# Optimization experiments

Hardware: AMD Instinct MI355X
Metric: run time of the kernel (lower is better)

## Reference

```python
import jax, jax.numpy as jnp
import numpy as np

B = 512       # number of graphs
MAX_N = 128   # pad length (>= max(num_atoms))
D = 256       # emb_dim


def setup_inputs() -> dict:
    key = jax.random.key(0)
    ks = jax.random.split(key, 20)
    num_atoms_np = np.full(B, 80, dtype=np.int64)
    num_atoms_np[: B // 2] = 112
    num_atoms_np[B // 2 :] = 48
    total = int(num_atoms_np.sum())  # 40960, static
    scale = 1.0 / np.sqrt(D)

    def lin_w(k):
        return jax.random.normal(k, (D, D), jnp.float32) * scale

    inp = {
        'rep_2d': jax.random.normal(ks[0], (total, D), jnp.float32),
        'rep_3d': jax.random.normal(ks[1], (total, D), jnp.float32),
        'num_atoms': jnp.asarray(num_atoms_np),
        # mha_2d_3d (queries from 2d, keys/values from 3d)
        'wq23': lin_w(ks[2]), 'bq23': jnp.zeros((D,), jnp.float32),
        'wk23': lin_w(ks[3]), 'bk23': jnp.zeros((D,), jnp.float32),
        'wv23': lin_w(ks[4]), 'bv23': jnp.zeros((D,), jnp.float32),
        # mha_3d_2d (queries from 3d, keys/values from 2d)
        'wq32': lin_w(ks[5]), 'bq32': jnp.zeros((D,), jnp.float32),
        'wk32': lin_w(ks[6]), 'bk32': jnp.zeros((D,), jnp.float32),
        'wv32': lin_w(ks[7]), 'bv32': jnp.zeros((D,), jnp.float32),
        # per-branch Linear (normalizer=Identity) + GELU
        'wm23': lin_w(ks[8]), 'bm23': jnp.zeros((D,), jnp.float32),
        'wm32': lin_w(ks[9]), 'bm32': jnp.zeros((D,), jnp.float32),
    }
    return inp


def _variadic_to_padded(flat, num_atoms):
    # flat: [total, D] -> padded [B, MAX_N, D], mask [B, MAX_N] (True = valid)
    cum = jnp.cumsum(num_atoms)
    offsets = cum - num_atoms
    pos = jnp.arange(MAX_N)
    mask = pos[None, :] < num_atoms[:, None]
    idx = jnp.where(mask, offsets[:, None] + pos[None, :], 0)
    padded = flat[idx] * mask[..., None].astype(flat.dtype)
    return padded, mask


def _padded_to_variadic(padded, num_atoms, total):
    # padded: [B, MAX_N, D] -> flat [total, D]
    cum = jnp.cumsum(num_atoms)
    t = jnp.arange(total)
    b = jnp.searchsorted(cum, t, side='right')
    i = t - (cum - num_atoms)[b]
    return padded[b, i]


def _cross_attn(q_in, kv_in, mask, wq, bq, wk, bk, wv, bv):
    # single-head scaled dot-product cross-attention, key-side padding mask
    q = q_in @ wq.T + bq
    k = kv_in @ wk.T + bk
    v = kv_in @ wv.T + bv
    s = jnp.einsum('bqd,bkd->bqk', q, k) / jnp.sqrt(jnp.asarray(D, q.dtype))
    s = jnp.where(mask[:, None, :], s, jnp.asarray(-1e9, s.dtype))
    a = jax.nn.softmax(s, axis=-1)
    return jnp.einsum('bqk,bkd->bqd', a, v)


def reference(rep_2d, rep_3d, num_atoms,
              wq23, bq23, wk23, bk23, wv23, bv23,
              wq32, bq32, wk32, bk32, wv32, bv32,
              wm23, bm23, wm32, bm32):
    total = rep_2d.shape[0]
    p2d, mask = _variadic_to_padded(rep_2d, num_atoms)
    p3d, _ = _variadic_to_padded(rep_3d, num_atoms)
    x2d = _cross_attn(p2d, p3d, mask, wq23, bq23, wk23, bk23, wv23, bv23)
    x3d = _cross_attn(p3d, p2d, mask, wq32, bq32, wk32, bk32, wv32, bv32)
    x2d = _padded_to_variadic(x2d, num_atoms, total)
    x3d = _padded_to_variadic(x3d, num_atoms, total)
    out2d = jax.nn.gelu(x2d @ wm23.T + bm23, approximate=False)
    out3d = jax.nn.gelu(x3d @ wm32.T + bm32, approximate=False)
    return (out2d, out3d)
```

## Files before the change

### kernel.cpp

```cpp
#include <hip/hip_runtime.h>
#include <hip/hip_bf16.h>
#include <cstdint>


typedef short s16x8 __attribute__((ext_vector_type(8)));
typedef float f32x4 __attribute__((ext_vector_type(4)));

__device__ __forceinline__ s16x8 cvt8(const float* p) {
  float4 a0 = *(const float4*)p, a1 = *(const float4*)(p + 4);
  union { s16x8 v; __bf16 e[8]; } u;
  u.e[0] = (__bf16)a0.x; u.e[1] = (__bf16)a0.y; u.e[2] = (__bf16)a0.z; u.e[3] = (__bf16)a0.w;
  u.e[4] = (__bf16)a1.x; u.e[5] = (__bf16)a1.y; u.e[6] = (__bf16)a1.z; u.e[7] = (__bf16)a1.w;
  return u.v;
}
__device__ __forceinline__ float fast_gelu(float x) {
  float ax = fabsf(x);
  float t = 1.0f / (1.0f + 0.3275911f * (ax * 0.70710678f));
  float y = t * (0.254829592f + t * (-0.284496736f + t * (1.421413741f +
            t * (-1.453152027f + t * 1.061405429f))));
  float er = 1.0f - y * __expf(-0.5f * ax * ax);
  er = (x < 0.f) ? -er : er;
  return 0.5f * x * (1.0f + er);
}

__global__ void sentinel_kernel(float* out, float v) {
  if (threadIdx.x == 0 && blockIdx.x == 0) out[0] = v;
}

__global__ __launch_bounds__(512) void scan_kernel(
    const int* __restrict__ na, int* __restrict__ offs,
    int B, int total, float* out)
{
  __shared__ int s32[512];
  __shared__ int s64[512];
  const int t = threadIdx.x;
  int v32 = 0, v64 = 0;
  if (t < B) {
    v32 = na[t];
    v64 = (int)((const long long*)na)[t];
  }
  s32[t] = v32; s64[t] = v64;
  __syncthreads();
  for (int o = 1; o < 512; o <<= 1) {
    int a = (t >= o) ? s32[t - o] : 0;
    int b = (t >= o) ? s64[t - o] : 0;
    __syncthreads();
    s32[t] += a; s64[t] += b;
    __syncthreads();
  }
  int tot32 = s32[B - 1], tot64 = s64[B - 1];
  bool ok32 = (tot32 == total), ok64 = (tot64 == total);
  if (t < B) offs[t] = ok32 ? (s32[t] - v32) : ok64 ? (s64[t] - v64) : 0;
  if (t == 0) {
    offs[B] = ok32 ? tot32 : ok64 ? tot64 : 0;
    if (!ok32 && !ok64) out[0] = 31337.0f;
  }
}

__global__ __launch_bounds__(256) void qkv_fused(
    const float* __restrict__ A,
    const float* __restrict__ Wq, const float* __restrict__ bq,
    const float* __restrict__ Wk, const float* __restrict__ bk,
    const float* __restrict__ Wv, const float* __restrict__ bv,
    __bf16* __restrict__ Qo, __bf16* __restrict__ Ko, __bf16* __restrict__ Vt,
    int total)
{
  __shared__ __bf16 Al[64][264];
  __shared__ __bf16 Wt[128][40];
  const int t = threadIdx.x, lane = t & 63, w = t >> 6;
  const int wr = w >> 1, wc = w & 1;
  const int l15 = lane & 15, l4 = lane >> 4;
  const int by = blockIdx.x;

  #pragma unroll
  for (int j = 0; j < 8; ++j) {
    int c = t + j * 256;
    int row = c >> 5, off0 = (c & 31) * 8;
    *(s16x8*)(&Al[row][off0]) = cvt8(A + (size_t)(by * 64 + row) * 256 + off0);
  }
  __syncthreads();

  #pragma unroll
  for (int wi = 0; wi < 3; ++wi) {
    const float* W  = (wi == 0) ? Wq : (wi == 1) ? Wk : Wv;
    const float* bs = (wi == 0) ? bq : (wi == 1) ? bk : bv;
    #pragma unroll
    for (int nx = 0; nx < 2; ++nx) {
      f32x4 acc[2][4];
      #pragma unroll
      for (int m = 0; m < 2; ++m)
        #pragma unroll
        for (int nn = 0; nn < 4; ++nn) acc[m][nn] = (f32x4){0.f, 0.f, 0.f, 0.f};

      for (int kk = 0; kk < 256; kk += 32) {
        __syncthreads();
        #pragma unroll
        for (int j = 0; j < 2; ++j) {
          int c = t + j * 256;
          int row = c >> 2, off0 = (c & 3) * 8;
          *(s16x8*)(&Wt[row][off0]) =
              cvt8(W + (size_t)(nx * 128 + row) * 256 + kk + off0);
        }
        __syncthreads();
        s16x8 af[2], bfr[4];
        #pragma unroll
        for (int m = 0; m < 2; ++m)
          af[m] = *(const s16x8*)(&Al[wr * 32 + m * 16 + l15][kk + l4 * 8]);
        #pragma unroll
        for (int nn = 0; nn < 4; ++nn)
          bfr[nn] = *(const s16x8*)(&Wt[wc * 64 + nn * 16 + l15][l4 * 8]);
        #pragma unroll
        for (int m = 0; m < 2; ++m)
          #pragma unroll
          for (int nn = 0; nn < 4; ++nn)
            acc[m][nn] = __builtin_amdgcn_mfma_f32_16x16x32_bf16(af[m], bfr[nn], acc[m][nn], 0, 0, 0);
      }

      if (wi < 2) {
        __bf16* O = (wi == 0) ? Qo : Ko;
        #pragma unroll
        for (int m = 0; m < 2; ++m) {
          int row0 = by * 64 + wr * 32 + m * 16 + l4 * 4;
          #pragma unroll
          for (int nn = 0; nn < 4; ++nn) {
            int col = nx * 128 + wc * 64 + nn * 16 + l15;
            float bc = bs[col];
            #pragma unroll
            for (int r = 0; r < 4; ++r)
              O[(size_t)(row0 + r) * 256 + col] = (__bf16)(acc[m][nn][r] + bc);
          }
        }
      } else {
        #pragma unroll
        for (int m = 0; m < 2; ++m) {
          int row0 = by * 64 + wr * 32 + m * 16 + l4 * 4;
          #pragma unroll
          for (int nn = 0; nn < 4; ++nn) {
            int col = nx * 128 + wc * 64 + nn * 16 + l15;
            float bc = bs[col];
            union { uint2 u; __bf16 e[4]; } pv;
            #pragma unroll
            for (int r = 0; r < 4; ++r) pv.e[r] = (__bf16)(acc[m][nn][r] + bc);
            *(uint2*)(&Vt[(size_t)col * total + row0]) = pv.u;
          }
        }
      }
    }
  }
}

__global__ __launch_bounds__(256) void gemm_kernel(
    const float* __restrict__ A, const float* __restrict__ Bw,
    const float* __restrict__ bias, __bf16* __restrict__ C,
    int N, int biasRow)
{
  __shared__ __bf16 At[128 * 32];
  __shared__ __bf16 Bt[128 * 32];
  const int t = threadIdx.x;
  const int lane = t & 63, w = t >> 6;
  const int wr = w >> 1, wc = w & 1;
  const int l15 = lane & 15, l4 = lane >> 4;
  const int by = blockIdx.x, bx = blockIdx.y;

  f32x4 acc[4][4];
  for (int m = 0; m < 4; ++m)
    for (int nn = 0; nn < 4; ++nn) acc[m][nn] = (f32x4){0.f, 0.f, 0.f, 0.f};

  for (int kk = 0; kk < 256; kk += 32) {
    for (int j = 0; j < 2; ++j) {
      int c = t + j * 256;
      int row = c >> 2, off0 = (c & 3) * 8;
      *(s16x8*)(&At[row * 32 + off0]) = cvt8(A + (size_t)(by * 128 + row) * 256 + kk + off0);
      *(s16x8*)(&Bt[row * 32 + off0]) = cvt8(Bw + (size_t)(bx * 128 + row) * 256 + kk + off0);
    }
    __syncthreads();
    s16x8 af[4], bfr[4];
    for (int m = 0; m < 4; ++m)
      af[m] = *(const s16x8*)(&At[(wr * 64 + m * 16 + l15) * 32 + l4 * 8]);
    for (int nn = 0; nn < 4; ++nn)
      bfr[nn] = *(const s16x8*)(&Bt[(wc * 64 + nn * 16 + l15) * 32 + l4 * 8]);
    for (int m = 0; m < 4; ++m)
      for (int nn = 0; nn < 4; ++nn)
        acc[m][nn] = __builtin_amdgcn_mfma_f32_16x16x32_bf16(af[m], bfr[nn], acc[m][nn], 0, 0, 0);
    __syncthreads();
  }

  for (int m = 0; m < 4; ++m) {
    int row0 = by * 128 + wr * 64 + m * 16 + l4 * 4;
    for (int nn = 0; nn < 4; ++nn) {
      int col = bx * 128 + wc * 64 + nn * 16 + l15;
      float bc = biasRow ? 0.f : bias[col];
      for (int r = 0; r < 4; ++r) {
        int row = row0 + r;
        float v = acc[m][nn][r] + (biasRow ? bias[row] : bc);
        C[(size_t)row * N + col] = (__bf16)v;
      }
    }
  }
}

__global__ __launch_bounds__(256) void gemm_out(
    const __bf16* __restrict__ A, const float* __restrict__ Bw,
    const float* __restrict__ bias, float* __restrict__ C, int N)
{
  __shared__ __bf16 At[64 * 32];
  __shared__ __bf16 Bt[128 * 32];
  const int t = threadIdx.x;
  const int lane = t & 63, w = t >> 6;
  const int wr = w >> 1, wc = w & 1;
  const int l15 = lane & 15, l4 = lane >> 4;
  const int by = blockIdx.x, bx = blockIdx.y;

  f32x4 acc[2][4];
  for (int m = 0; m < 2; ++m)
    for (int nn = 0; nn < 4; ++nn) acc[m][nn] = (f32x4){0.f, 0.f, 0.f, 0.f};

  for (int kk = 0; kk < 256; kk += 32) {
    {
      int row = t >> 2, off0 = (t & 3) * 8;
      *(s16x8*)(&At[row * 32 + off0]) =
          *(const s16x8*)(A + (size_t)(by * 64 + row) * 256 + kk + off0);
    }
    for (int j = 0; j < 2; ++j) {
      int c = t + j * 256;
      int row = c >> 2, off0 = (c & 3) * 8;
      *(s16x8*)(&Bt[row * 32 + off0]) = cvt8(Bw + (size_t)(bx * 128 + row) * 256 + kk + off0);
    }
    __syncthreads();
    s16x8 af[2], bfr[4];
    for (int m = 0; m < 2; ++m)
      af[m] = *(const s16x8*)(&At[(wr * 32 + m * 16 + l15) * 32 + l4 * 8]);
    for (int nn = 0; nn < 4; ++nn)
      bfr[nn] = *(const s16x8*)(&Bt[(wc * 64 + nn * 16 + l15) * 32 + l4 * 8]);
    for (int m = 0; m < 2; ++m)
      for (int nn = 0; nn < 4; ++nn)
        acc[m][nn] = __builtin_amdgcn_mfma_f32_16x16x32_bf16(af[m], bfr[nn], acc[m][nn], 0, 0, 0);
    __syncthreads();
  }

  for (int m = 0; m < 2; ++m) {
    int row0 = by * 64 + wr * 32 + m * 16 + l4 * 4;
    for (int nn = 0; nn < 4; ++nn) {
      int col = bx * 128 + wc * 64 + nn * 16 + l15;
      float bc = bias[col];
      for (int r = 0; r < 4; ++r) {
        int row = row0 + r;
        C[(size_t)row * N + col] = fast_gelu(acc[m][nn][r] + bc);
      }
    }
  }
}

#define KSTR 264
#define PSTR 136
__global__ __launch_bounds__(512, 2) void attn_kernel(
    const __bf16* __restrict__ Q, const __bf16* __restrict__ Km,
    const __bf16* __restrict__ Vt, __bf16* __restrict__ X,
    const int* __restrict__ offs, int total)
{
  __shared__ __bf16 smem[128 * KSTR];
  __bf16 (*Klds)[KSTR] = (__bf16(*)[KSTR])smem;
  __bf16 (*Plds)[PSTR] = (__bf16(*)[PSTR])smem;

  const int g = blockIdx.x;
  const int off = offs[g];
  const int n = offs[g + 1] - off;
  const int t = threadIdx.x, lane = t & 63, w = t >> 6;
  const int l15 = lane & 15, l4 = lane >> 4;
  const bool qact = (w * 16) < n;

  uint4 kst[8];
  #pragma unroll
  for (int j = 0; j < 8; ++j) {
    int row = j * 16 + (t >> 5);
    kst[j] = *(const uint4*)((const char*)(Km + (size_t)(off + row) * 256) + (t & 31) * 16);
  }
  s16x8 qf[8];
  if (qact) {
    int qr = w * 16 + l15; if (qr >= n) qr = n - 1;
    const __bf16* qp = Q + (size_t)(off + qr) * 256 + l4 * 8;
    #pragma unroll
    for (int kk = 0; kk < 8; ++kk) qf[kk] = *(const s16x8*)(qp + kk * 32);
  }
  #pragma unroll
  for (int j = 0; j < 8; ++j) {
    int row = j * 16 + (t >> 5);
    *(uint4*)((char*)&Klds[row][0] + (t & 31) * 16) = kst[j];
  }
  __syncthreads();

  f32x4 sacc[8];
  #pragma unroll
  for (int i = 0; i < 8; ++i) sacc[i] = (f32x4){0.f, 0.f, 0.f, 0.f};
  if (qact) {
    #pragma unroll
    for (int kt = 0; kt < 8; ++kt) {
      if (kt * 16 < n) {
        const __bf16* kp = &Klds[kt * 16 + l15][l4 * 8];
        #pragma unroll
        for (int kk = 0; kk < 8; ++kk) {
          s16x8 kf = *(const s16x8*)(kp + kk * 32);
          sacc[kt] = __builtin_amdgcn_mfma_f32_16x16x32_bf16(qf[kk], kf, sacc[kt], 0, 0, 0);
        }
      }
    }
  }
  __syncthreads();

  if (qact) {
    #pragma unroll
    for (int r = 0; r < 4; ++r) {
      float sv[8];
      float m = -1e30f;
      #pragma unroll
      for (int kt = 0; kt < 8; ++kt) {
        int key = kt * 16 + l15;
        float v = (key < n) ? sacc[kt][r] * 0.0625f : -1e30f;
        sv[kt] = v; m = fmaxf(m, v);
      }
      for (int o = 1; o < 16; o <<= 1) m = fmaxf(m, __shfl_xor(m, o));
      float p[8], sum = 0.f;
      #pragma unroll
      for (int kt = 0; kt < 8; ++kt) { p[kt] = __expf(sv[kt] - m); sum += p[kt]; }
      for (int o = 1; o < 16; o <<= 1) sum += __shfl_xor(sum, o);
      float inv = 1.f / sum;
      int q = w * 16 + l4 * 4 + r;
      #pragma unroll
      for (int kt = 0; kt < 8; ++kt)
        Plds[q][kt * 16 + l15] = (__bf16)(p[kt] * inv);
    }
  }
  __syncthreads();

  const int dbase = w * 32;
  f32x4 xacc[2][8];
  #pragma unroll
  for (int dt = 0; dt < 2; ++dt)
    #pragma unroll
    for (int qm = 0; qm < 8; ++qm) xacc[dt][qm] = (f32x4){0.f, 0.f, 0.f, 0.f};

  #pragma unroll
  for (int dt = 0; dt < 2; ++dt) {
    int d = dbase + dt * 16 + l15;
    s16x8 vf[4];
    #pragma unroll
    for (int ks = 0; ks < 4; ++ks) {
      int kc = off + ks * 32 + l4 * 8;
      if (kc > total - 8) kc = total - 8;
      vf[ks] = *(const s16x8*)(Vt + (size_t)d * total + kc);
    }
    #pragma unroll
    for (int qm = 0; qm < 8; ++qm) {
      #pragma unroll
      for (int ks = 0; ks < 4; ++ks) {
        if (ks * 32 < n) {
          s16x8 pa = *(const s16x8*)(&Plds[qm * 16 + l15][ks * 32 + l4 * 8]);
          xacc[dt][qm] = __builtin_amdgcn_mfma_f32_16x16x32_bf16(pa, vf[ks], xacc[dt][qm], 0, 0, 0);
        }
      }
    }
  }

  #pragma unroll
  for (int dt = 0; dt < 2; ++dt)
    #pragma unroll
    for (int qm = 0; qm < 8; ++qm)
      #pragma unroll
      for (int r = 0; r < 4; ++r) {
        int q = qm * 16 + l4 * 4 + r;
        if (q < n)
          X[(size_t)(off + q) * 256 + dbase + dt * 16 + l15] = (__bf16)xacc[dt][qm][r];
      }
}

extern "C" void kernel_launch(void* const* d_in, const int* in_sizes, int n_in,
                              void* d_out, int out_size, void* d_ws, size_t ws_size,
                              hipStream_t stream) {
  const float* rep2d = (const float*)d_in[0];
  const float* rep3d = (const float*)d_in[1];
  const int*   na    = (const int*)d_in[2];
  const float* wq23 = (const float*)d_in[3];  const float* bq23 = (const float*)d_in[4];
  const float* wk23 = (const float*)d_in[5];  const float* bk23 = (const float*)d_in[6];
  const float* wv23 = (const float*)d_in[7];  const float* bv23 = (const float*)d_in[8];
  const float* wq32 = (const float*)d_in[9];  const float* bq32 = (const float*)d_in[10];
  const float* wk32 = (const float*)d_in[11]; const float* bk32 = (const float*)d_in[12];
  const float* wv32 = (const float*)d_in[13]; const float* bv32 = (const float*)d_in[14];
  const float* wm23 = (const float*)d_in[15]; const float* bm23 = (const float*)d_in[16];
  const float* wm32 = (const float*)d_in[17]; const float* bm32 = (const float*)d_in[18];

  const int B = in_sizes[2];
  const int total = in_sizes[0] / 256;
  float* out = (float*)d_out;

  char* ws = (char*)d_ws;
  const size_t SZ = (size_t)total * 256 * sizeof(__bf16);
  const size_t need6 = 8192 + 6 * SZ;
  const size_t need3 = 8192 + 3 * SZ;
  int* offs = (int*)ws;

  dim3 blk(256);
  dim3 gO(total / 64, 2);
  dim3 gA(B);
  dim3 blkA(512);

  if (ws_size >= need6) {
    __bf16* BQ1 = (__bf16*)(ws + 8192);
    __bf16* BK1 = (__bf16*)(ws + 8192 + SZ);
    __bf16* BV1 = (__bf16*)(ws + 8192 + 2 * SZ);
    __bf16* BQ2 = (__bf16*)(ws + 8192 + 3 * SZ);
    __bf16* BK2 = (__bf16*)(ws + 8192 + 4 * SZ);
    __bf16* BV2 = (__bf16*)(ws + 8192 + 5 * SZ);

    scan_kernel<<<1, 512, 0, stream>>>(na, offs, B, total, out);
    qkv_fused<<<total / 64, blk, 0, stream>>>(rep2d, wq23, bq23, wk32, bk32,
                                              wv32, bv32, BQ1, BK2, BV2, total);
    qkv_fused<<<total / 64, blk, 0, stream>>>(rep3d, wq32, bq32, wk23, bk23,
                                              wv23, bv23, BQ2, BK1, BV1, total);
    attn_kernel<<<gA, blkA, 0, stream>>>(BQ1, BK1, BV1, BQ1, offs, total);
    gemm_out<<<gO, blk, 0, stream>>>(BQ1, wm23, bm23, out, 256);
    attn_kernel<<<gA, blkA, 0, stream>>>(BQ2, BK2, BV2, BQ2, offs, total);
    gemm_out<<<gO, blk, 0, stream>>>(BQ2, wm32, bm32, out + (size_t)total * 256, 256);
  } else if (ws_size >= need3) {
    __bf16* BQ = (__bf16*)(ws + 8192);
    __bf16* BK = (__bf16*)(ws + 8192 + SZ);
    __bf16* BV = (__bf16*)(ws + 8192 + 2 * SZ);
    dim3 gP(total / 128, 2);
    dim3 gV(2, total / 128);

    scan_kernel<<<1, 512, 0, stream>>>(na, offs, B, total, out);
    gemm_kernel<<<gP, blk, 0, stream>>>(rep2d, wq23, bq23, BQ, 256, 0);
    gemm_kernel<<<gP, blk, 0, stream>>>(rep3d, wk23, bk23, BK, 256, 0);
    gemm_kernel<<<gV, blk, 0, stream>>>(wv23, rep3d, bv23, BV, total, 1);
    attn_kernel<<<gA, blkA, 0, stream>>>(BQ, BK, BV, BQ, offs, total);
    gemm_out<<<gO, blk, 0, stream>>>(BQ, wm23, bm23, out, 256);
    gemm_kernel<<<gP, blk, 0, stream>>>(rep3d, wq32, bq32, BQ, 256, 0);
    gemm_kernel<<<gP, blk, 0, stream>>>(rep2d, wk32, bk32, BK, 256, 0);
    gemm_kernel<<<gV, blk, 0, stream>>>(wv32, rep2d, bv32, BV, total, 1);
    attn_kernel<<<gA, blkA, 0, stream>>>(BQ, BK, BV, BQ, offs, total);
    gemm_out<<<gO, blk, 0, stream>>>(BQ, wm32, bm32, out + (size_t)total * 256, 256);
  } else {
    sentinel_kernel<<<1, 64, 0, stream>>>(out, 54321.0f);
  }
}
```

Before: 216.0 us.

## Pre-convert QKV weights to bf16 and load MFMA fragments directly from global

Adds a small kernel that converts the six QKV weight matrices to bf16 once per call into workspace. The QKV kernel drops its shared-memory staging. Activation fragments are converted straight into registers, and weight fragments are read directly from the bf16 global copy, which removes the per-k-step barriers and repeated fp32-to-bf16 conversion of weights in every block. The trade is one extra launch, more register pressure, and uncoalesced-ish 16-byte global loads for weights that now rely on L2/cache instead of LDS.

```diff
diff --git a/kernel.cpp b/kernel.cpp
--- a/kernel.cpp
+++ b/kernel.cpp
@@ -57,32 +57,44 @@
   }
 }
 
+__global__ __launch_bounds__(256) void cvt6_kernel(
+    const float* __restrict__ w0, const float* __restrict__ w1,
+    const float* __restrict__ w2, const float* __restrict__ w3,
+    const float* __restrict__ w4, const float* __restrict__ w5,
+    __bf16* __restrict__ out)
+{
+  const int wi = blockIdx.y;
+  const float* w = (wi == 0) ? w0 : (wi == 1) ? w1 : (wi == 2) ? w2
+                 : (wi == 3) ? w3 : (wi == 4) ? w4 : w5;
+  int i = (blockIdx.x * 256 + threadIdx.x) * 4;
+  float4 f = *(const float4*)(w + i);
+  __bf16* o = out + (size_t)wi * 65536 + i;
+  o[0] = (__bf16)f.x; o[1] = (__bf16)f.y; o[2] = (__bf16)f.z; o[3] = (__bf16)f.w;
+}
+
 __global__ __launch_bounds__(256) void qkv_fused(
-    const float* __restrict__ A,
-    const float* __restrict__ Wq, const float* __restrict__ bq,
-    const float* __restrict__ Wk, const float* __restrict__ bk,
-    const float* __restrict__ Wv, const float* __restrict__ bv,
+    const float* __restrict__ A, const __bf16* __restrict__ Wb,
+    const float* __restrict__ bq, const float* __restrict__ bk,
+    const float* __restrict__ bv,
     __bf16* __restrict__ Qo, __bf16* __restrict__ Ko, __bf16* __restrict__ Vt,
     int total)
 {
-  __shared__ __bf16 Al[64][264];
-  __shared__ __bf16 Wt[128][40];
   const int t = threadIdx.x, lane = t & 63, w = t >> 6;
   const int wr = w >> 1, wc = w & 1;
   const int l15 = lane & 15, l4 = lane >> 4;
   const int by = blockIdx.x;
 
-  #pragma unroll
-  for (int j = 0; j < 8; ++j) {
-    int c = t + j * 256;
-    int row = c >> 5, off0 = (c & 31) * 8;
-    *(s16x8*)(&Al[row][off0]) = cvt8(A + (size_t)(by * 64 + row) * 256 + off0);
-  }
-  __syncthreads();
+  s16x8 afr[2][8];
+  #pragma unroll
+  for (int m = 0; m < 2; ++m) {
+    const float* ap = A + (size_t)(by * 64 + wr * 32 + m * 16 + l15) * 256 + l4 * 8;
+    #pragma unroll
+    for (int kk = 0; kk < 8; ++kk) afr[m][kk] = cvt8(ap + kk * 32);
+  }
 
   #pragma unroll
   for (int wi = 0; wi < 3; ++wi) {
-    const float* W  = (wi == 0) ? Wq : (wi == 1) ? Wk : Wv;
+    const __bf16* W  = Wb + (size_t)wi * 65536;
     const float* bs = (wi == 0) ? bq : (wi == 1) ? bk : bv;
     #pragma unroll
     for (int nx = 0; nx < 2; ++nx) {
@@ -92,28 +104,18 @@
         #pragma unroll
         for (int nn = 0; nn < 4; ++nn) acc[m][nn] = (f32x4){0.f, 0.f, 0.f, 0.f};
 
-      for (int kk = 0; kk < 256; kk += 32) {
-        __syncthreads();
-        #pragma unroll
-        for (int j = 0; j < 2; ++j) {
-          int c = t + j * 256;
-          int row = c >> 2, off0 = (c & 3) * 8;
-          *(s16x8*)(&Wt[row][off0]) =
-              cvt8(W + (size_t)(nx * 128 + row) * 256 + kk + off0);
-        }
-        __syncthreads();
-        s16x8 af[2], bfr[4];
-        #pragma unroll
-        for (int m = 0; m < 2; ++m)
-          af[m] = *(const s16x8*)(&Al[wr * 32 + m * 16 + l15][kk + l4 * 8]);
+      #pragma unroll
+      for (int kk = 0; kk < 8; ++kk) {
+        s16x8 wf[4];
         #pragma unroll
         for (int nn = 0; nn < 4; ++nn)
-          bfr[nn] = *(const s16x8*)(&Wt[wc * 64 + nn * 16 + l15][l4 * 8]);
+          wf[nn] = *(const s16x8*)(W + (size_t)(nx * 128 + wc * 64 + nn * 16 + l15) * 256
+                                    + kk * 32 + l4 * 8);
         #pragma unroll
         for (int m = 0; m < 2; ++m)
           #pragma unroll
           for (int nn = 0; nn < 4; ++nn)
-            acc[m][nn] = __builtin_amdgcn_mfma_f32_16x16x32_bf16(af[m], bfr[nn], acc[m][nn], 0, 0, 0);
+            acc[m][nn] = __builtin_amdgcn_mfma_f32_16x16x32_bf16(afr[m][kk], wf[nn], acc[m][nn], 0, 0, 0);
       }
 
       if (wi < 2) {
@@ -394,7 +396,8 @@
 
   char* ws = (char*)d_ws;
   const size_t SZ = (size_t)total * 256 * sizeof(__bf16);
-  const size_t need6 = 8192 + 6 * SZ;
+  const size_t WB = 6 * 65536 * sizeof(__bf16);
+  const size_t need6 = 8192 + WB + 6 * SZ;
   const size_t need3 = 8192 + 3 * SZ;
   int* offs = (int*)ws;
 
@@ -404,18 +407,20 @@
   dim3 blkA(512);
 
   if (ws_size >= need6) {
-    __bf16* BQ1 = (__bf16*)(ws + 8192);
-    __bf16* BK1 = (__bf16*)(ws + 8192 + SZ);
-    __bf16* BV1 = (__bf16*)(ws + 8192 + 2 * SZ);
-    __bf16* BQ2 = (__bf16*)(ws + 8192 + 3 * SZ);
-    __bf16* BK2 = (__bf16*)(ws + 8192 + 4 * SZ);
-    __bf16* BV2 = (__bf16*)(ws + 8192 + 5 * SZ);
+    __bf16* WBp = (__bf16*)(ws + 8192);
+    __bf16* BQ1 = (__bf16*)(ws + 8192 + WB);
+    __bf16* BK1 = (__bf16*)(ws + 8192 + WB + SZ);
+    __bf16* BV1 = (__bf16*)(ws + 8192 + WB + 2 * SZ);
+    __bf16* BQ2 = (__bf16*)(ws + 8192 + WB + 3 * SZ);
+    __bf16* BK2 = (__bf16*)(ws + 8192 + WB + 4 * SZ);
+    __bf16* BV2 = (__bf16*)(ws + 8192 + WB + 5 * SZ);
 
     scan_kernel<<<1, 512, 0, stream>>>(na, offs, B, total, out);
-    qkv_fused<<<total / 64, blk, 0, stream>>>(rep2d, wq23, bq23, wk32, bk32,
-                                              wv32, bv32, BQ1, BK2, BV2, total);
-    qkv_fused<<<total / 64, blk, 0, stream>>>(rep3d, wq32, bq32, wk23, bk23,
-                                              wv23, bv23, BQ2, BK1, BV1, total);
+    cvt6_kernel<<<dim3(64, 6), blk, 0, stream>>>(wq23, wk32, wv32, wq32, wk23, wv23, WBp);
+    qkv_fused<<<total / 64, blk, 0, stream>>>(rep2d, WBp, bq23, bk32, bv32,
+                                              BQ1, BK2, BV2, total);
+    qkv_fused<<<total / 64, blk, 0, stream>>>(rep3d, WBp + 3 * 65536, bq32, bk23, bv23,
+                                              BQ2, BK1, BV1, total);
     attn_kernel<<<gA, blkA, 0, stream>>>(BQ1, BK1, BV1, BQ1, offs, total);
     gemm_out<<<gO, blk, 0, stream>>>(BQ1, wm23, bm23, out, 256);
     attn_kernel<<<gA, blkA, 0, stream>>>(BQ2, BK2, BV2, BQ2, offs, total);
```

Result: slower. 274.5 us (+27.1%).

## Batch both branches into single projection, attention, and output launches

Applied to the files above, without the earlier changes.

Replaces the two per-input fused QKV kernels with one 3D-grid projection kernel that runs all six Q/K/V GEMMs as independent 128x128 tiles. The attention and output GEMMs for both branches are merged into single launches indexed by blockIdx.y/z. The aim is fewer launches, more blocks in flight per launch, and no serialization between the two branches. In exchange, the A-tile reuse across Q/K/V in the old fused kernel is lost: each input tile is reloaded and reconverted for every projection, and the grid includes early-exit blocks.

```diff
diff --git a/kernel.cpp b/kernel.cpp
--- a/kernel.cpp
+++ b/kernel.cpp
@@ -57,93 +57,253 @@
   }
 }
 
-__global__ __launch_bounds__(256) void qkv_fused(
-    const float* __restrict__ A,
-    const float* __restrict__ Wq, const float* __restrict__ bq,
-    const float* __restrict__ Wk, const float* __restrict__ bk,
-    const float* __restrict__ Wv, const float* __restrict__ bv,
-    __bf16* __restrict__ Qo, __bf16* __restrict__ Ko, __bf16* __restrict__ Vt,
-    int total)
+struct Proj6Args {
+  const float* A[6]; const float* W[6]; const float* bias[6];
+  unsigned long long C[6];
+};
+__global__ __launch_bounds__(256) void proj6_kernel(Proj6Args args, int total)
 {
-  __shared__ __bf16 Al[64][264];
-  __shared__ __bf16 Wt[128][40];
-  const int t = threadIdx.x, lane = t & 63, w = t >> 6;
+  __shared__ __bf16 At[128 * 32];
+  __shared__ __bf16 Bt[128 * 32];
+  const int z = blockIdx.z;
+  const bool vcase = (z == 2 || z == 5);
+  const float* A  = args.A[z];
+  const float* Bw = args.W[z];
+  const float* bs = args.bias[z];
+  __bf16* C = (__bf16*)args.C[z];
+  const int N = vcase ? total : 256;
+  const int by = vcase ? blockIdx.y : blockIdx.x;
+  const int bx = vcase ? blockIdx.x : blockIdx.y;
+  if (vcase && blockIdx.x >= (unsigned)(total / 128)) return;
+  if (!vcase && blockIdx.y >= 2) return;
+
+  const int t = threadIdx.x;
+  const int lane = t & 63, w = t >> 6;
   const int wr = w >> 1, wc = w & 1;
   const int l15 = lane & 15, l4 = lane >> 4;
-  const int by = blockIdx.x;
-
+
+  f32x4 acc[4][4];
+  for (int m = 0; m < 4; ++m)
+    for (int nn = 0; nn < 4; ++nn) acc[m][nn] = (f32x4){0.f, 0.f, 0.f, 0.f};
+
+  for (int kk = 0; kk < 256; kk += 32) {
+    for (int j = 0; j < 2; ++j) {
+      int c = t + j * 256;
+      int row = c >> 2, off0 = (c & 3) * 8;
+      *(s16x8*)(&At[row * 32 + off0]) = cvt8(A + (size_t)(by * 128 + row) * 256 + kk + off0);
+      *(s16x8*)(&Bt[row * 32 + off0]) = cvt8(Bw + (size_t)(bx * 128 + row) * 256 + kk + off0);
+    }
+    __syncthreads();
+    s16x8 af[4], bfr[4];
+    for (int m = 0; m < 4; ++m)
+      af[m] = *(const s16x8*)(&At[(wr * 64 + m * 16 + l15) * 32 + l4 * 8]);
+    for (int nn = 0; nn < 4; ++nn)
+      bfr[nn] = *(const s16x8*)(&Bt[(wc * 64 + nn * 16 + l15) * 32 + l4 * 8]);
+    for (int m = 0; m < 4; ++m)
+      for (int nn = 0; nn < 4; ++nn)
+        acc[m][nn] = __builtin_amdgcn_mfma_f32_16x16x32_bf16(af[m], bfr[nn], acc[m][nn], 0, 0, 0);
+    __syncthreads();
+  }
+
+  for (int m = 0; m < 4; ++m) {
+    int row0 = by * 128 + wr * 64 + m * 16 + l4 * 4;
+    for (int nn = 0; nn < 4; ++nn) {
+      int col = bx * 128 + wc * 64 + nn * 16 + l15;
+      float bc = vcase ? 0.f : bs[col];
+      for (int r = 0; r < 4; ++r) {
+        int row = row0 + r;
+        float v = acc[m][nn][r] + (vcase ? bs[row] : bc);
+        C[(size_t)row * N + col] = (__bf16)v;
+      }
+    }
+  }
+}
+
+struct Attn2Args {
+  const __bf16* Q[2]; const __bf16* K[2]; const __bf16* V[2];
+  unsigned long long X[2];
+};
+#define KSTR 264
+#define PSTR 136
+__global__ __launch_bounds__(512, 2) void attn2_kernel(
+    Attn2Args args, const int* __restrict__ offs, int total)
+{
+  __shared__ __bf16 smem[128 * KSTR];
+  __bf16 (*Klds)[KSTR] = (__bf16(*)[KSTR])smem;
+  __bf16 (*Plds)[PSTR] = (__bf16(*)[PSTR])smem;
+
+  const int br = blockIdx.y;
+  const __bf16* Q  = args.Q[br];
+  const __bf16* Km = args.K[br];
+  const __bf16* Vt = args.V[br];
+  __bf16* X = (__bf16*)args.X[br];
+
+  const int g = blockIdx.x;
+  const int off = offs[g];
+  const int n = offs[g + 1] - off;
+  const int t = threadIdx.x, lane = t & 63, w = t >> 6;
+  const int l15 = lane & 15, l4 = lane >> 4;
+  const bool qact = (w * 16) < n;
+
+  uint4 kst[8];
   #pragma unroll
   for (int j = 0; j < 8; ++j) {
-    int c = t + j * 256;
-    int row = c >> 5, off0 = (c & 31) * 8;
-    *(s16x8*)(&Al[row][off0]) = cvt8(A + (size_t)(by * 64 + row) * 256 + off0);
+    int row = j * 16 + (t >> 5);
+    kst[j] = *(const uint4*)((const char*)(Km + (size_t)(off + row) * 256) + (t & 31) * 16);
+  }
+  s16x8 qf[8];
+  if (qact) {
+    int qr = w * 16 + l15; if (qr >= n) qr = n - 1;
+    const __bf16* qp = Q + (size_t)(off + qr) * 256 + l4 * 8;
+    #pragma unroll
+    for (int kk = 0; kk < 8; ++kk) qf[kk] = *(const s16x8*)(qp + kk * 32);
+  }
+  #pragma unroll
+  for (int j = 0; j < 8; ++j) {
+    int row = j * 16 + (t >> 5);
+    *(uint4*)((char*)&Klds[row][0] + (t & 31) * 16) = kst[j];
   }
   __syncthreads();
 
-  #pragma unroll
-  for (int wi = 0; wi < 3; ++wi) {
-    const float* W  = (wi == 0) ? Wq : (wi == 1) ? Wk : Wv;
-    const float* bs = (wi == 0) ? bq : (wi == 1) ? bk : bv;
-    #pragma unroll
-    for (int nx = 0; nx < 2; ++nx) {
-      f32x4 acc[2][4];
+  f32x4 sacc[8];
+  #pragma unroll
+  for (int i = 0; i < 8; ++i) sacc[i] = (f32x4){0.f, 0.f, 0.f, 0.f};
+  if (qact) {
+    #pragma unroll
+    for (int kt = 0; kt < 8; ++kt) {
+      if (kt * 16 < n) {
+        const __bf16* kp = &Klds[kt * 16 + l15][l4 * 8];
+        #pragma unroll
+        for (int kk = 0; kk < 8; ++kk) {
+          s16x8 kf = *(const s16x8*)(kp + kk * 32);
+          sacc[kt] = __builtin_amdgcn_mfma_f32_16x16x32_bf16(qf[kk], kf, sacc[kt], 0, 0, 0);
+        }
+      }
+    }
+  }
+  __syncthreads();
+
+  if (qact) {
+    #pragma unroll
+    for (int r = 0; r < 4; ++r) {
+      float sv[8];
+      float m = -1e30f;
       #pragma unroll
-      for (int m = 0; m < 2; ++m)
-        #pragma unroll
-        for (int nn = 0; nn < 4; ++nn) acc[m][nn] = (f32x4){0.f, 0.f, 0.f, 0.f};
-
-      for (int kk = 0; kk < 256; kk += 32) {
-        __syncthreads();
-        #pragma unroll
-        for (int j = 0; j < 2; ++j) {
-          int c = t + j * 256;
-          int row = c >> 2, off0 = (c & 3) * 8;
-          *(s16x8*)(&Wt[row][off0]) =
-              cvt8(W + (size_t)(nx * 128 + row) * 256 + kk + off0);
+      for (int kt = 0; kt < 8; ++kt) {
+        int key = kt * 16 + l15;
+        float v = (key < n) ? sacc[kt][r] * 0.0625f : -1e30f;
+        sv[kt] = v; m = fmaxf(m, v);
+      }
+      for (int o = 1; o < 16; o <<= 1) m = fmaxf(m, __shfl_xor(m, o));
+      float p[8], sum = 0.f;
+      #pragma unroll
+      for (int kt = 0; kt < 8; ++kt) { p[kt] = __expf(sv[kt] - m); sum += p[kt]; }
+      for (int o = 1; o < 16; o <<= 1) sum += __shfl_xor(sum, o);
+      float inv = 1.f / sum;
+      int q = w * 16 + l4 * 4 + r;
+      #pragma unroll
+      for (int kt = 0; kt < 8; ++kt)
+        Plds[q][kt * 16 + l15] = (__bf16)(p[kt] * inv);
+    }
+  }
+  __syncthreads();
+
+  const int dbase = w * 32;
+  f32x4 xacc[2][8];
+  #pragma unroll
+  for (int dt = 0; dt < 2; ++dt)
+    #pragma unroll
+    for (int qm = 0; qm < 8; ++qm) xacc[dt][qm] = (f32x4){0.f, 0.f, 0.f, 0.f};
+
+  #pragma unroll
+  for (int dt = 0; dt < 2; ++dt) {
+    int d = dbase + dt * 16 + l15;
+    s16x8 vf[4];
+    #pragma unroll
+    for (int ks = 0; ks < 4; ++ks) {
+      int kc = off + ks * 32 + l4 * 8;
+      if (kc > total - 8) kc = total - 8;
+      vf[ks] = *(const s16x8*)(Vt + (size_t)d * total + kc);
+    }
+    #pragma unroll
+    for (int qm = 0; qm < 8; ++qm) {
+      #pragma unroll
+      for (int ks = 0; ks < 4; ++ks) {
+        if (ks * 32 < n) {
+          s16x8 pa = *(const s16x8*)(&Plds[qm * 16 + l15][ks * 32 + l4 * 8]);
+          xacc[dt][qm] = __builtin_amdgcn_mfma_f32_16x16x32_bf16(pa, vf[ks], xacc[dt][qm], 0, 0, 0);
         }
-        __syncthreads();
-        s16x8 af[2], bfr[4];
-        #pragma unroll
-        for (int m = 0; m < 2; ++m)
-          af[m] = *(const s16x8*)(&Al[wr * 32 + m * 16 + l15][kk + l4 * 8]);
-        #pragma unroll
-        for (int nn = 0; nn < 4; ++nn)
-          bfr[nn] = *(const s16x8*)(&Wt[wc * 64 + nn * 16 + l15][l4 * 8]);
-        #pragma unroll
-        for (int m = 0; m < 2; ++m)
-          #pragma unroll
-          for (int nn = 0; nn < 4; ++nn)
-            acc[m][nn] = __builtin_amdgcn_mfma_f32_16x16x32_bf16(af[m], bfr[nn], acc[m][nn], 0, 0, 0);
-      }
-
-      if (wi < 2) {
-        __bf16* O = (wi == 0) ? Qo : Ko;
-        #pragma unroll
-        for (int m = 0; m < 2; ++m) {
-          int row0 = by * 64 + wr * 32 + m * 16 + l4 * 4;
-          #pragma unroll
-          for (int nn = 0; nn < 4; ++nn) {
-            int col = nx * 128 + wc * 64 + nn * 16 + l15;
-            float bc = bs[col];
-            #pragma unroll
-            for (int r = 0; r < 4; ++r)
-              O[(size_t)(row0 + r) * 256 + col] = (__bf16)(acc[m][nn][r] + bc);
-          }
-        }
-      } else {
-        #pragma unroll
-        for (int m = 0; m < 2; ++m) {
-          int row0 = by * 64 + wr * 32 + m * 16 + l4 * 4;
-          #pragma unroll
-          for (int nn = 0; nn < 4; ++nn) {
-            int col = nx * 128 + wc * 64 + nn * 16 + l15;
-            float bc = bs[col];
-            union { uint2 u; __bf16 e[4]; } pv;
-            #pragma unroll
-            for (int r = 0; r < 4; ++r) pv.e[r] = (__bf16)(acc[m][nn][r] + bc);
-            *(uint2*)(&Vt[(size_t)col * total + row0]) = pv.u;
-          }
-        }
+      }
+    }
+  }
+
+  #pragma unroll
+  for (int dt = 0; dt < 2; ++dt)
+    #pragma unroll
+    for (int qm = 0; qm < 8; ++qm)
+      #pragma unroll
+      for (int r = 0; r < 4; ++r) {
+        int q = qm * 16 + l4 * 4 + r;
+        if (q < n)
+          X[(size_t)(off + q) * 256 + dbase + dt * 16 + l15] = (__bf16)xacc[dt][qm][r];
+      }
+}
+
+struct Out2Args {
+  const __bf16* A[2]; const float* W[2]; const float* bias[2];
+  unsigned long long C[2];
+};
+__global__ __launch_bounds__(256) void gemm_out2(Out2Args args)
+{
+  __shared__ __bf16 At[64 * 32];
+  __shared__ __bf16 Bt[128 * 32];
+  const int z = blockIdx.z;
+  const __bf16* A  = args.A[z];
+  const float* Bw  = args.W[z];
+  const float* bias = args.bias[z];
+  float* C = (float*)args.C[z];
+
+  const int t = threadIdx.x;
+  const int lane = t & 63, w = t >> 6;
+  const int wr = w >> 1, wc = w & 1;
+  const int l15 = lane & 15, l4 = lane >> 4;
+  const int by = blockIdx.x, bx = blockIdx.y;
+
+  f32x4 acc[2][4];
+  for (int m = 0; m < 2; ++m)
+    for (int nn = 0; nn < 4; ++nn) acc[m][nn] = (f32x4){0.f, 0.f, 0.f, 0.f};
+
+  for (int kk = 0; kk < 256; kk += 32) {
+    {
+      int row = t >> 2, off0 = (t & 3) * 8;
+      *(s16x8*)(&At[row * 32 + off0]) =
+          *(const s16x8*)(A + (size_t)(by * 64 + row) * 256 + kk + off0);
+    }
+    for (int j = 0; j < 2; ++j) {
+      int c = t + j * 256;
+      int row = c >> 2, off0 = (c & 3) * 8;
+      *(s16x8*)(&Bt[row * 32 + off0]) = cvt8(Bw + (size_t)(bx * 128 + row) * 256 + kk + off0);
+    }
+    __syncthreads();
+    s16x8 af[2], bfr[4];
+    for (int m = 0; m < 2; ++m)
+      af[m] = *(const s16x8*)(&At[(wr * 32 + m * 16 + l15) * 32 + l4 * 8]);
+    for (int nn = 0; nn < 4; ++nn)
+      bfr[nn] = *(const s16x8*)(&Bt[(wc * 64 + nn * 16 + l15) * 32 + l4 * 8]);
+    for (int m = 0; m < 2; ++m)
+      for (int nn = 0; nn < 4; ++nn)
+        acc[m][nn] = __builtin_amdgcn_mfma_f32_16x16x32_bf16(af[m], bfr[nn], acc[m][nn], 0, 0, 0);
+    __syncthreads();
+  }
+
+  for (int m = 0; m < 2; ++m) {
+    int row0 = by * 64 + wr * 32 + m * 16 + l4 * 4;
+    for (int nn = 0; nn < 4; ++nn) {
+      int col = bx * 128 + wc * 64 + nn * 16 + l15;
+      float bc = bias[col];
+      for (int r = 0; r < 4; ++r) {
+        int row = row0 + r;
+        C[(size_t)row * 256 + col] = fast_gelu(acc[m][nn][r] + bc);
       }
     }
   }
@@ -197,180 +357,6 @@
       }
     }
   }
-}
-
-__global__ __launch_bounds__(256) void gemm_out(
-    const __bf16* __restrict__ A, const float* __restrict__ Bw,
-    const float* __restrict__ bias, float* __restrict__ C, int N)
-{
-  __shared__ __bf16 At[64 * 32];
-  __shared__ __bf16 Bt[128 * 32];
-  const int t = threadIdx.x;
-  const int lane = t & 63, w = t >> 6;
-  const int wr = w >> 1, wc = w & 1;
-  const int l15 = lane & 15, l4 = lane >> 4;
-  const int by = blockIdx.x, bx = blockIdx.y;
-
-  f32x4 acc[2][4];
-  for (int m = 0; m < 2; ++m)
-    for (int nn = 0; nn < 4; ++nn) acc[m][nn] = (f32x4){0.f, 0.f, 0.f, 0.f};
-
-  for (int kk = 0; kk < 256; kk += 32) {
-    {
-      int row = t >> 2, off0 = (t & 3) * 8;
-      *(s16x8*)(&At[row * 32 + off0]) =
-          *(const s16x8*)(A + (size_t)(by * 64 + row) * 256 + kk + off0);
-    }
-    for (int j = 0; j < 2; ++j) {
-      int c = t + j * 256;
-      int row = c >> 2, off0 = (c & 3) * 8;
-      *(s16x8*)(&Bt[row * 32 + off0]) = cvt8(Bw + (size_t)(bx * 128 + row) * 256 + kk + off0);
-    }
-    __syncthreads();
-    s16x8 af[2], bfr[4];
-    for (int m = 0; m < 2; ++m)
-      af[m] = *(const s16x8*)(&At[(wr * 32 + m * 16 + l15) * 32 + l4 * 8]);
-    for (int nn = 0; nn < 4; ++nn)
-      bfr[nn] = *(const s16x8*)(&Bt[(wc * 64 + nn * 16 + l15) * 32 + l4 * 8]);
-    for (int m = 0; m < 2; ++m)
-      for (int nn = 0; nn < 4; ++nn)
-        acc[m][nn] = __builtin_amdgcn_mfma_f32_16x16x32_bf16(af[m], bfr[nn], acc[m][nn], 0, 0, 0);
-    __syncthreads();
-  }
-
-  for (int m = 0; m < 2; ++m) {
-    int row0 = by * 64 + wr * 32 + m * 16 + l4 * 4;
-    for (int nn = 0; nn < 4; ++nn) {
-      int col = bx * 128 + wc * 64 + nn * 16 + l15;
-      float bc = bias[col];
-      for (int r = 0; r < 4; ++r) {
-        int row = row0 + r;
-        C[(size_t)row * N + col] = fast_gelu(acc[m][nn][r] + bc);
-      }
-    }
-  }
-}
-
-#define KSTR 264
-#define PSTR 136
-__global__ __launch_bounds__(512, 2) void attn_kernel(
-    const __bf16* __restrict__ Q, const __bf16* __restrict__ Km,
-    const __bf16* __restrict__ Vt, __bf16* __restrict__ X,
-    const int* __restrict__ offs, int total)
-{
-  __shared__ __bf16 smem[128 * KSTR];
-  __bf16 (*Klds)[KSTR] = (__bf16(*)[KSTR])smem;
-  __bf16 (*Plds)[PSTR] = (__bf16(*)[PSTR])smem;
-
-  const int g = blockIdx.x;
-  const int off = offs[g];
-  const int n = offs[g + 1] - off;
-  const int t = threadIdx.x, lane = t & 63, w = t >> 6;
-  const int l15 = lane & 15, l4 = lane >> 4;
-  const bool qact = (w * 16) < n;
-
-  uint4 kst[8];
-  #pragma unroll
-  for (int j = 0; j < 8; ++j) {
-    int row = j * 16 + (t >> 5);
-    kst[j] = *(const uint4*)((const char*)(Km + (size_t)(off + row) * 256) + (t & 31) * 16);
-  }
-  s16x8 qf[8];
-  if (qact) {
-    int qr = w * 16 + l15; if (qr >= n) qr = n - 1;
-    const __bf16* qp = Q + (size_t)(off + qr) * 256 + l4 * 8;
-    #pragma unroll
-    for (int kk = 0; kk < 8; ++kk) qf[kk] = *(const s16x8*)(qp + kk * 32);
-  }
-  #pragma unroll
-  for (int j = 0; j < 8; ++j) {
-    int row = j * 16 + (t >> 5);
-    *(uint4*)((char*)&Klds[row][0] + (t & 31) * 16) = kst[j];
-  }
-  __syncthreads();
-
-  f32x4 sacc[8];
-  #pragma unroll
-  for (int i = 0; i < 8; ++i) sacc[i] = (f32x4){0.f, 0.f, 0.f, 0.f};
-  if (qact) {
-    #pragma unroll
-    for (int kt = 0; kt < 8; ++kt) {
-      if (kt * 16 < n) {
-        const __bf16* kp = &Klds[kt * 16 + l15][l4 * 8];
-        #pragma unroll
-        for (int kk = 0; kk < 8; ++kk) {
-          s16x8 kf = *(const s16x8*)(kp + kk * 32);
-          sacc[kt] = __builtin_amdgcn_mfma_f32_16x16x32_bf16(qf[kk], kf, sacc[kt], 0, 0, 0);
-        }
-      }
-    }
-  }
-  __syncthreads();
-
-  if (qact) {
-    #pragma unroll
-    for (int r = 0; r < 4; ++r) {
-      float sv[8];
-      float m = -1e30f;
-      #pragma unroll
-      for (int kt = 0; kt < 8; ++kt) {
-        int key = kt * 16 + l15;
-        float v = (key < n) ? sacc[kt][r] * 0.0625f : -1e30f;
-        sv[kt] = v; m = fmaxf(m, v);
-      }
-      for (int o = 1; o < 16; o <<= 1) m = fmaxf(m, __shfl_xor(m, o));
-      float p[8], sum = 0.f;
-      #pragma unroll
-      for (int kt = 0; kt < 8; ++kt) { p[kt] = __expf(sv[kt] - m); sum += p[kt]; }
-      for (int o = 1; o < 16; o <<= 1) sum += __shfl_xor(sum, o);
-      float inv = 1.f / sum;
-      int q = w * 16 + l4 * 4 + r;
-      #pragma unroll
-      for (int kt = 0; kt < 8; ++kt)
-        Plds[q][kt * 16 + l15] = (__bf16)(p[kt] * inv);
-    }
-  }
-  __syncthreads();
-
-  const int dbase = w * 32;
-  f32x4 xacc[2][8];
-  #pragma unroll
-  for (int dt = 0; dt < 2; ++dt)
-    #pragma unroll
-    for (int qm = 0; qm < 8; ++qm) xacc[dt][qm] = (f32x4){0.f, 0.f, 0.f, 0.f};
-
-  #pragma unroll
-  for (int dt = 0; dt < 2; ++dt) {
-    int d = dbase + dt * 16 + l15;
-    s16x8 vf[4];
-    #pragma unroll
-    for (int ks = 0; ks < 4; ++ks) {
-      int kc = off + ks * 32 + l4 * 8;
-      if (kc > total - 8) kc = total - 8;
-      vf[ks] = *(const s16x8*)(Vt + (size_t)d * total + kc);
-    }
-    #pragma unroll
-    for (int qm = 0; qm < 8; ++qm) {
-      #pragma unroll
-      for (int ks = 0; ks < 4; ++ks) {
-        if (ks * 32 < n) {
-          s16x8 pa = *(const s16x8*)(&Plds[qm * 16 + l15][ks * 32 + l4 * 8]);
-          xacc[dt][qm] = __builtin_amdgcn_mfma_f32_16x16x32_bf16(pa, vf[ks], xacc[dt][qm], 0, 0, 0);
-        }
-      }
-    }
-  }
-
-  #pragma unroll
-  for (int dt = 0; dt < 2; ++dt)
-    #pragma unroll
-    for (int qm = 0; qm < 8; ++qm)
-      #pragma unroll
-      for (int r = 0; r < 4; ++r) {
-        int q = qm * 16 + l4 * 4 + r;
-        if (q < n)
-          X[(size_t)(off + q) * 256 + dbase + dt * 16 + l15] = (__bf16)xacc[dt][qm][r];
-      }
 }
 
 extern "C" void kernel_launch(void* const* d_in, const int* in_sizes, int n_in,
@@ -399,8 +385,6 @@
   int* offs = (int*)ws;
 
   dim3 blk(256);
-  dim3 gO(total / 64, 2);
-  dim3 gA(B);
   dim3 blkA(512);
 
   if (ws_size >= need6) {
@@ -412,32 +396,56 @@
     __bf16* BV2 = (__bf16*)(ws + 8192 + 5 * SZ);
 
     scan_kernel<<<1, 512, 0, stream>>>(na, offs, B, total, out);
-    qkv_fused<<<total / 64, blk, 0, stream>>>(rep2d, wq23, bq23, wk32, bk32,
-                                              wv32, bv32, BQ1, BK2, BV2, total);
-    qkv_fused<<<total / 64, blk, 0, stream>>>(rep3d, wq32, bq32, wk23, bk23,
-                                              wv23, bv23, BQ2, BK1, BV1, total);
-    attn_kernel<<<gA, blkA, 0, stream>>>(BQ1, BK1, BV1, BQ1, offs, total);
-    gemm_out<<<gO, blk, 0, stream>>>(BQ1, wm23, bm23, out, 256);
-    attn_kernel<<<gA, blkA, 0, stream>>>(BQ2, BK2, BV2, BQ2, offs, total);
-    gemm_out<<<gO, blk, 0, stream>>>(BQ2, wm32, bm32, out + (size_t)total * 256, 256);
+
+    Proj6Args pa;
+    pa.A[0] = rep2d; pa.W[0] = wq23; pa.bias[0] = bq23; pa.C[0] = (unsigned long long)BQ1;
+    pa.A[1] = rep3d; pa.W[1] = wk23; pa.bias[1] = bk23; pa.C[1] = (unsigned long long)BK1;
+    pa.A[2] = wv23;  pa.W[2] = rep3d; pa.bias[2] = bv23; pa.C[2] = (unsigned long long)BV1;
+    pa.A[3] = rep3d; pa.W[3] = wq32; pa.bias[3] = bq32; pa.C[3] = (unsigned long long)BQ2;
+    pa.A[4] = rep2d; pa.W[4] = wk32; pa.bias[4] = bk32; pa.C[4] = (unsigned long long)BK2;
+    pa.A[5] = wv32;  pa.W[5] = rep2d; pa.bias[5] = bv32; pa.C[5] = (unsigned long long)BV2;
+    proj6_kernel<<<dim3(total / 128, 2, 6), blk, 0, stream>>>(pa, total);
+
+    Attn2Args aa;
+    aa.Q[0] = BQ1; aa.K[0] = BK1; aa.V[0] = BV1; aa.X[0] = (unsigned long long)BQ1;
+    aa.Q[1] = BQ2; aa.K[1] = BK2; aa.V[1] = BV2; aa.X[1] = (unsigned long long)BQ2;
+    attn2_kernel<<<dim3(B, 2), blkA, 0, stream>>>(aa, offs, total);
+
+    Out2Args oa;
+    oa.A[0] = BQ1; oa.W[0] = wm23; oa.bias[0] = bm23; oa.C[0] = (unsigned long long)out;
+    oa.A[1] = BQ2; oa.W[1] = wm32; oa.bias[1] = bm32;
+    oa.C[1] = (unsigned long long)(out + (size_t)total * 256);
+    gemm_out2<<<dim3(total / 64, 2, 2), blk, 0, stream>>>(oa);
   } else if (ws_size >= need3) {
     __bf16* BQ = (__bf16*)(ws + 8192);
     __bf16* BK = (__bf16*)(ws + 8192 + SZ);
     __bf16* BV = (__bf16*)(ws + 8192 + 2 * SZ);
     dim3 gP(total / 128, 2);
     dim3 gV(2, total / 128);
+    dim3 gA(B);
 
     scan_kernel<<<1, 512, 0, stream>>>(na, offs, B, total, out);
-    gemm_kernel<<<gP, blk, 0, stream>>>(rep2d, wq23, bq23, BQ, 256, 0);
-    gemm_kernel<<<gP, blk, 0, stream>>>(rep3d, wk23, bk23, BK, 256, 0);
-    gemm_kernel<<<gV, blk, 0, stream>>>(wv23, rep3d, bv23, BV, total, 1);
-    attn_kernel<<<gA, blkA, 0, stream>>>(BQ, BK, BV, BQ, offs, total);
-    gemm_out<<<gO, blk, 0, stream>>>(BQ, wm23, bm23, out, 256);
-    gemm_kernel<<<gP, blk, 0, stream>>>(rep3d, wq32, bq32, BQ, 256, 0);
-    gemm_kernel<<<gP, blk, 0, stream>>>(rep2d, wk32, bk32, BK, 256, 0);
-    gemm_kernel<<<gV, blk, 0, stream>>>(wv32, rep2d, bv32, BV, total, 1);
-    attn_kernel<<<gA, blkA, 0, stream>>>(BQ, BK, BV, BQ, offs, total);
-    gemm_out<<<gO, blk, 0, stream>>>(BQ, wm32, bm32, out + (size_t)total * 256, 256);
+    for (int br = 0; br < 2; ++br) {
+      const float* rq = br ? rep3d : rep2d;
+      const float* rk = br ? rep2d : rep3d;
+      const float* wq = br ? wq32 : wq23;  const float* bq = br ? bq32 : bq23;
+      const float* wk = br ? wk32 : wk23;  const float* bk = br ? bk32 : bk23;
+      const float* wv = br ? wv32 : wv23;  const float* bv = br ? bv32 : bv23;
+      const float* wm = br ? wm32 : wm23;  const float* bm = br ? bm32 : bm23;
+      float* o = out + (size_t)br * total * 256;
+
+      gemm_kernel<<<gP, blk, 0, stream>>>(rq, wq, bq, BQ, 256, 0);
+      gemm_kernel<<<gP, blk, 0, stream>>>(rk, wk, bk, BK, 256, 0);
+      gemm_kernel<<<gV, blk, 0, stream>>>(wv, rk, bv, BV, total, 1);
+      Attn2Args aa;
+      aa.Q[0] = BQ; aa.K[0] = BK; aa.V[0] = BV; aa.X[0] = (unsigned long long)BQ;
+      aa.Q[1] = BQ; aa.K[1] = BK; aa.V[1] = BV; aa.X[1] = (unsigned long long)BQ;
+      attn2_kernel<<<dim3(B, 1), blkA, 0, stream>>>(aa, offs, total);
+      Out2Args oa;
+      oa.A[0] = BQ; oa.W[0] = wm; oa.bias[0] = bm; oa.C[0] = (unsigned long long)o;
+      oa.A[1] = BQ; oa.W[1] = wm; oa.bias[1] = bm; oa.C[1] = (unsigned long long)o;
+      gemm_out2<<<dim3(total / 64, 2, 1), blk, 0, stream>>>(oa);
+    }
   } else {
     sentinel_kernel<<<1, 64, 0, stream>>>(out, 54321.0f);
   }
```

Result: slower. 238.7 us (+10.5%).
